# Optimization experiments

Measured on AMD Instinct MI355X. Metric: run time of the kernel, lower is better.

The kernel has to match this reference:

```python
import jax, jax.numpy as jnp
import numpy as np
from jax import lax

N, H, W = 16, 112, 112
CIN, COUT, K = 256, 256, 3
STRIDE, PAD = 1, 1


def setup_inputs() -> dict:
    key = jax.random.key(0)
    kx, kw = jax.random.split(key)
    # int8-valued activations and weights, stored as int32 for portable integer conv
    x = jax.random.randint(kx, (N, H, W, CIN), -128, 128, dtype=jnp.int32)
    # weight layout matches the torch module: (out_channels, kH, kW, in_channels) == OHWI
    weight = jax.random.randint(kw, (COUT, K, K, CIN), -128, 128, dtype=jnp.int32)
    return {"x": x, "weight": weight}


def reference(x, weight):
    y = lax.conv_general_dilated(
        x,
        weight,
        window_strides=(STRIDE, STRIDE),
        padding=[(PAD, PAD), (PAD, PAD)],
        dimension_numbers=("NHWC", "OHWI", "NHWC"),
        preferred_element_type=jnp.int32,
    )
    return y  # (N, H, W, COUT) int32
```

## Files before the change

### kernel.cpp

```cpp
#include <hip/hip_runtime.h>
#include <stdint.h>

#define NN   16
#define HH   112
#define WW   112
#define CIN  256
#define COUT 256
#define HP   114
#define WP   114
#define M_TOTAL (NN * HH * WW)
#define XP_BYTES ((size_t)NN * HP * WP * CIN)
#define WPK_BYTES ((size_t)9 * COUT * CIN)

typedef int v4i __attribute__((ext_vector_type(4)));

__device__ __forceinline__ void load_lds16(const void* g, void* l) {
  __builtin_amdgcn_global_load_lds(
      (const __attribute__((address_space(1))) void*)g,
      (__attribute__((address_space(3))) void*)l, 16, 0, 0);
}

__device__ __forceinline__ void bar() {
  asm volatile("" ::: "memory");
  __builtin_amdgcn_s_barrier();
  asm volatile("" ::: "memory");
}

__device__ __forceinline__ int pack4(int a, int b, int c, int d) {
  return (a & 255) | ((b & 255) << 8) | ((c & 255) << 16) | (d << 24);
}

__global__ void pack_x_kernel(const int* __restrict__ x, char* __restrict__ xp) {
  int t = blockIdx.x * 256 + threadIdx.x;
  int g = t & 15;
  int p = t >> 4;
  int w = p % WW;
  int t2 = p / WW;
  int h = t2 % HH;
  int n = t2 / HH;
  const int4* src = (const int4*)(x + (size_t)t * 16);
  int4 a = src[0], b = src[1], c = src[2], d = src[3];
  int4 ov;
  ov.x = pack4(a.x, a.y, a.z, a.w);
  ov.y = pack4(b.x, b.y, b.z, b.w);
  ov.z = pack4(c.x, c.y, c.z, c.w);
  ov.w = pack4(d.x, d.y, d.z, d.w);
  size_t dst = (((size_t)n * HP + (h + 1)) * WP + (w + 1)) * CIN + (size_t)g * 16;
  *(int4*)(xp + dst) = ov;
}

__global__ void pack_w_border_kernel(const int* __restrict__ wgt, char* __restrict__ xp,
                                     char* __restrict__ wp) {
  int bid = blockIdx.x;
  if (bid < 576) {
    int t = bid * 256 + threadIdx.x;
    int c4 = t & 63;
    int r = t >> 6;
    int tap = r % 9;
    int cout = r / 9;
    int4 v = *(const int4*)(wgt + (size_t)t * 4);
    int ov = pack4(v.x, v.y, v.z, v.w);
    size_t dst = ((size_t)tap * COUT + cout) * CIN + (size_t)c4 * 4;
    *(int*)(wp + dst) = ov;
  } else {
    int t = (bid - 576) * 256 + threadIdx.x;
    int g = t & 15;
    int pix = t >> 4;
    int n = pix / 452;
    int b = pix % 452;
    int h, w;
    if (b < 114) { h = 0; w = b; }
    else if (b < 228) { h = 113; w = b - 114; }
    else { int r = b - 228; h = 1 + (r >> 1); w = (r & 1) ? 113 : 0; }
    size_t dst = (((size_t)n * HP + h) * WP + w) * CIN + (size_t)g * 16;
    *(int4*)(xp + dst) = make_int4(0, 0, 0, 0);
  }
}

__global__ __launch_bounds__(256, 2) void conv_mfma_kernel(const char* __restrict__ xp,
                                                           const char* __restrict__ wp,
                                                           int* __restrict__ out) {
  __shared__ __align__(16) char Bs[3 * 256 * 64];
  const int tid = threadIdx.x;
  const int lane = tid & 63;
  const int wave = tid >> 6;
  const int mtile = blockIdx.x;
  const int wm = wave & 1;
  const int wn = wave >> 1;

  const char* gptrB[4];
  char* lptrB[4];
#pragma unroll
  for (int j = 0; j < 4; j++) {
    int c = wave * 4 + j;
    int row = c * 16 + (lane >> 2);
    int colg = (lane & 3) ^ ((row >> 1) & 3);
    gptrB[j] = wp + (size_t)row * CIN + (size_t)colg * 16;
    lptrB[j] = Bs + c * 1024;
  }

  const char* abase[4];
#pragma unroll
  for (int i = 0; i < 4; i++) {
    int ra = mtile * 128 + wm * 64 + i * 16 + (lane & 15);
    int w = ra % WW;
    int t2 = ra / WW;
    int h = t2 % HH;
    int n = t2 / HH;
    abase[i] = xp + (((size_t)n * HP + h) * WP + w) * CIN + (size_t)(lane >> 4) * 16;
  }

  int boff[8];
#pragma unroll
  for (int j = 0; j < 8; j++) {
    int rb = wn * 128 + j * 16 + (lane & 15);
    boff[j] = rb * 64 + (((lane >> 4) ^ ((rb >> 1) & 3)) * 16);
  }

  v4i acc[4][8];
#pragma unroll
  for (int i = 0; i < 4; i++)
#pragma unroll
    for (int j = 0; j < 8; j++) acc[i][j] = (v4i){0, 0, 0, 0};

  auto stageB = [&](int ks, int b) {
    int tap = ks >> 2;
    int kb = ks & 3;
    int offB = tap * (COUT * CIN) + kb * 64;
#pragma unroll
    for (int j = 0; j < 4; j++) load_lds16(gptrB[j] + offB, lptrB[j] + b * 16384);
  };
  auto gatherA = [&](int ks, v4i* dst) {
    int tap = ks >> 2;
    int kb = ks & 3;
    int ky = tap / 3;
    int kx = tap - ky * 3;
    int off = (ky * WP + kx) * CIN + kb * 64;
#pragma unroll
    for (int i = 0; i < 4; i++) dst[i] = *(const v4i*)(abase[i] + off);
  };

  v4i afr[2][4];

  stageB(0, 0);
  stageB(1, 1);
  gatherA(0, afr[0]);
  asm volatile("s_waitcnt vmcnt(8)" ::: "memory");
  bar();

#define CONV_STEP(KS, BC, CUR, NXT, DOSTAGE, DOGATHER, VMN)                         \
  {                                                                                 \
    const char* Bb = Bs + (BC) * 16384;                                             \
    v4i bf[8];                                                                      \
    _Pragma("unroll") for (int j = 0; j < 8; j++)                                   \
        bf[j] = *(const v4i*)(Bb + boff[j]);                                        \
    if (DOSTAGE) stageB((KS) + 2, ((BC) + 2) % 3);                                  \
    if (DOGATHER) gatherA((KS) + 1, afr[NXT]);                                      \
    asm volatile("s_waitcnt vmcnt(" VMN ")" ::: "memory");                          \
    __builtin_amdgcn_s_setprio(1);                                                  \
    _Pragma("unroll") for (int i = 0; i < 4; i++)                                   \
      _Pragma("unroll") for (int j = 0; j < 8; j++)                                 \
        acc[i][j] = __builtin_amdgcn_mfma_i32_16x16x64_i8(afr[CUR][i], bf[j],       \
                                                          acc[i][j], 0, 0, 0);      \
    __builtin_amdgcn_s_setprio(0);                                                  \
    bar();                                                                          \
  }

#pragma unroll 1
  for (int it = 0; it < 5; it++) {
    int base = it * 6;
#pragma unroll
    for (int u = 0; u < 6; u++) {
      CONV_STEP(base + u, u % 3, u & 1, (u + 1) & 1, true, true, "8")
    }
  }
  CONV_STEP(30, 0, 0, 1, true,  true,  "8")
  CONV_STEP(31, 1, 1, 0, true,  true,  "8")
  CONV_STEP(32, 2, 0, 1, true,  true,  "8")
  CONV_STEP(33, 0, 1, 0, true,  true,  "8")
  CONV_STEP(34, 1, 0, 1, false, true,  "4")
  CONV_STEP(35, 2, 1, 0, false, false, "0")
#undef CONV_STEP

#pragma unroll
  for (int i = 0; i < 4; i++) {
    const int mg = mtile * 128 + wm * 64 + i * 16 + ((lane >> 4) * 4);
#pragma unroll
    for (int r = 0; r < 4; r++) {
      int* orow = out + (size_t)(mg + r) * COUT + wn * 128 + (lane & 15);
#pragma unroll
      for (int j = 0; j < 8; j++) orow[j * 16] = acc[i][j][r];
    }
  }
}

__global__ void conv_naive_kernel(const int* __restrict__ x, const int* __restrict__ wgt,
                                  int* __restrict__ out, int total) {
  int idx = blockIdx.x * 256 + threadIdx.x;
  if (idx >= total) return;
  int co = idx & 255;
  int p = idx >> 8;
  int w = p % WW;
  int t2 = p / WW;
  int h = t2 % HH;
  int n = t2 / HH;
  int acc = 0;
  for (int ky = 0; ky < 3; ky++) {
    int ih = h + ky - 1;
    if (ih < 0 || ih >= HH) continue;
    for (int kx = 0; kx < 3; kx++) {
      int iw = w + kx - 1;
      if (iw < 0 || iw >= WW) continue;
      const int* xs = x + (((size_t)n * HH + ih) * WW + iw) * CIN;
      const int* ws = wgt + ((size_t)co * 9 + ky * 3 + kx) * CIN;
      for (int ci = 0; ci < CIN; ci++) acc += xs[ci] * ws[ci];
    }
  }
  out[idx] = acc;
}

extern "C" void kernel_launch(void* const* d_in, const int* in_sizes, int n_in,
                              void* d_out, int out_size, void* d_ws, size_t ws_size,
                              hipStream_t stream) {
  const int* x = (const int*)d_in[0];
  const int* wgt = (const int*)d_in[1];
  int* out = (int*)d_out;
  const size_t need = XP_BYTES + WPK_BYTES;
  if (ws_size >= need) {
    char* xp = (char*)d_ws;
    char* wp = xp + XP_BYTES;
    pack_x_kernel<<<(M_TOTAL * 16) / 256, 256, 0, stream>>>(x, xp);
    pack_w_border_kernel<<<576 + 452, 256, 0, stream>>>(wgt, xp, wp);
    conv_mfma_kernel<<<M_TOTAL / 128, 256, 0, stream>>>(xp, wp, out);
  } else {
    conv_naive_kernel<<<(out_size + 255) / 256, 256, 0, stream>>>(x, wgt, out, out_size);
  }
}
```

Baseline: 571.3 us.

## Enlarge conv tile to 256x256 with LDS-staged A and 4-deep pipeline

The conv kernel moves from 128-row tiles with 4 waves to 256-row by 256-column tiles with 8 waves. Both the im2col A tile and the B weights are now staged into LDS with direct global-to-LDS loads through a 4-buffer ring, replacing per-lane global gathers of A. Each wave computes 128x64 in two halves with extra barriers between them. The two pack kernels are merged into one launch. The aim is more data reuse per block and less global A traffic, at the cost of more LDS use (128KB), more barriers and possibly lower occupancy.

Result: faster. 473.1 us (-17.2%).

```diff
diff --git a/kernel.cpp b/kernel.cpp
--- a/kernel.cpp
+++ b/kernel.cpp
@@ -20,40 +20,34 @@
       (__attribute__((address_space(3))) void*)l, 16, 0, 0);
 }
 
-__device__ __forceinline__ void bar() {
-  asm volatile("" ::: "memory");
-  __builtin_amdgcn_s_barrier();
-  asm volatile("" ::: "memory");
-}
-
 __device__ __forceinline__ int pack4(int a, int b, int c, int d) {
   return (a & 255) | ((b & 255) << 8) | ((c & 255) << 16) | (d << 24);
 }
 
-__global__ void pack_x_kernel(const int* __restrict__ x, char* __restrict__ xp) {
-  int t = blockIdx.x * 256 + threadIdx.x;
-  int g = t & 15;
-  int p = t >> 4;
-  int w = p % WW;
-  int t2 = p / WW;
-  int h = t2 % HH;
-  int n = t2 / HH;
-  const int4* src = (const int4*)(x + (size_t)t * 16);
-  int4 a = src[0], b = src[1], c = src[2], d = src[3];
-  int4 ov;
-  ov.x = pack4(a.x, a.y, a.z, a.w);
-  ov.y = pack4(b.x, b.y, b.z, b.w);
-  ov.z = pack4(c.x, c.y, c.z, c.w);
-  ov.w = pack4(d.x, d.y, d.z, d.w);
-  size_t dst = (((size_t)n * HP + (h + 1)) * WP + (w + 1)) * CIN + (size_t)g * 16;
-  *(int4*)(xp + dst) = ov;
-}
-
-__global__ void pack_w_border_kernel(const int* __restrict__ wgt, char* __restrict__ xp,
-                                     char* __restrict__ wp) {
+__global__ __launch_bounds__(256) void pack_all_kernel(const int* __restrict__ x,
+                                                       const int* __restrict__ wgt,
+                                                       char* __restrict__ xp,
+                                                       char* __restrict__ wp) {
   int bid = blockIdx.x;
-  if (bid < 576) {
+  if (bid < 12544) {
     int t = bid * 256 + threadIdx.x;
+    int g = t & 15;
+    int p = t >> 4;
+    int w = p % WW;
+    int t2 = p / WW;
+    int h = t2 % HH;
+    int n = t2 / HH;
+    const int4* src = (const int4*)(x + (size_t)t * 16);
+    int4 a = src[0], b = src[1], c = src[2], d = src[3];
+    int4 ov;
+    ov.x = pack4(a.x, a.y, a.z, a.w);
+    ov.y = pack4(b.x, b.y, b.z, b.w);
+    ov.z = pack4(c.x, c.y, c.z, c.w);
+    ov.w = pack4(d.x, d.y, d.z, d.w);
+    size_t dst = (((size_t)n * HP + (h + 1)) * WP + (w + 1)) * CIN + (size_t)g * 16;
+    *(int4*)(xp + dst) = ov;
+  } else if (bid < 12544 + 576) {
+    int t = (bid - 12544) * 256 + threadIdx.x;
     int c4 = t & 63;
     int r = t >> 6;
     int tap = r % 9;
@@ -63,7 +57,7 @@
     size_t dst = ((size_t)tap * COUT + cout) * CIN + (size_t)c4 * 4;
     *(int*)(wp + dst) = ov;
   } else {
-    int t = (bid - 576) * 256 + threadIdx.x;
+    int t = (bid - 13120) * 256 + threadIdx.x;
     int g = t & 15;
     int pix = t >> 4;
     int n = pix / 452;
@@ -77,10 +71,11 @@
   }
 }
 
-__global__ __launch_bounds__(256, 2) void conv_mfma_kernel(const char* __restrict__ xp,
+__global__ __launch_bounds__(512, 2) void conv_mfma_kernel(const char* __restrict__ xp,
                                                            const char* __restrict__ wp,
                                                            int* __restrict__ out) {
-  __shared__ __align__(16) char Bs[3 * 256 * 64];
+  __shared__ __align__(16) char As[4 * 16384];
+  __shared__ __align__(16) char Bs[4 * 16384];
   const int tid = threadIdx.x;
   const int lane = tid & 63;
   const int wave = tid >> 6;
@@ -88,108 +83,121 @@
   const int wm = wave & 1;
   const int wn = wave >> 1;
 
-  const char* gptrB[4];
-  char* lptrB[4];
+  const int rA0 = (tid >> 2);
+  const int rA1 = 128 + (tid >> 2);
+  const int gcA0 = (tid & 3) ^ ((rA0 >> 1) & 3);
+  const int gcA1 = (tid & 3) ^ ((rA1 >> 1) & 3);
+  const char *gsrcA0, *gsrcA1;
+  {
+    int m0 = mtile * 256 + rA0;
+    int w0 = m0 % WW; int q0 = m0 / WW; int h0 = q0 % HH; int n0 = q0 / HH;
+    gsrcA0 = xp + (((size_t)n0 * HP + h0) * WP + w0) * CIN + (size_t)gcA0 * 16;
+    int m1 = mtile * 256 + rA1;
+    int w1 = m1 % WW; int q1 = m1 / WW; int h1 = q1 % HH; int n1 = q1 / HH;
+    gsrcA1 = xp + (((size_t)n1 * HP + h1) * WP + w1) * CIN + (size_t)gcA1 * 16;
+  }
+  const char* gsrcB0 = wp + (size_t)rA0 * CIN + (size_t)gcA0 * 16;
+  const char* gsrcB1 = wp + (size_t)rA1 * CIN + (size_t)gcA1 * 16;
+
+  int aoff[8], boff[4];
+#pragma unroll
+  for (int i = 0; i < 8; i++) {
+    int r = wm * 128 + i * 16 + (lane & 15);
+    aoff[i] = r * 64 + (((lane >> 4) ^ ((r >> 1) & 3)) * 16);
+  }
 #pragma unroll
   for (int j = 0; j < 4; j++) {
-    int c = wave * 4 + j;
-    int row = c * 16 + (lane >> 2);
-    int colg = (lane & 3) ^ ((row >> 1) & 3);
-    gptrB[j] = wp + (size_t)row * CIN + (size_t)colg * 16;
-    lptrB[j] = Bs + c * 1024;
-  }
-
-  const char* abase[4];
-#pragma unroll
-  for (int i = 0; i < 4; i++) {
-    int ra = mtile * 128 + wm * 64 + i * 16 + (lane & 15);
-    int w = ra % WW;
-    int t2 = ra / WW;
-    int h = t2 % HH;
-    int n = t2 / HH;
-    abase[i] = xp + (((size_t)n * HP + h) * WP + w) * CIN + (size_t)(lane >> 4) * 16;
-  }
-
-  int boff[8];
-#pragma unroll
-  for (int j = 0; j < 8; j++) {
-    int rb = wn * 128 + j * 16 + (lane & 15);
+    int rb = wn * 64 + j * 16 + (lane & 15);
     boff[j] = rb * 64 + (((lane >> 4) ^ ((rb >> 1) & 3)) * 16);
   }
 
-  v4i acc[4][8];
-#pragma unroll
-  for (int i = 0; i < 4; i++)
-#pragma unroll
-    for (int j = 0; j < 8; j++) acc[i][j] = (v4i){0, 0, 0, 0};
-
-  auto stageB = [&](int ks, int b) {
-    int tap = ks >> 2;
-    int kb = ks & 3;
-    int offB = tap * (COUT * CIN) + kb * 64;
-#pragma unroll
-    for (int j = 0; j < 4; j++) load_lds16(gptrB[j] + offB, lptrB[j] + b * 16384);
+  v4i acc[8][4];
+#pragma unroll
+  for (int i = 0; i < 8; i++)
+#pragma unroll
+    for (int j = 0; j < 4; j++) acc[i][j] = (v4i){0, 0, 0, 0};
+
+  auto stage = [&](int oA, int oB, int buf) {
+    char* Adst = As + buf * 16384 + wave * 1024;
+    char* Bdst = Bs + buf * 16384 + wave * 1024;
+    load_lds16(gsrcA0 + oA, Adst);
+    load_lds16(gsrcA1 + oA, Adst + 8192);
+    load_lds16(gsrcB0 + oB, Bdst);
+    load_lds16(gsrcB1 + oB, Bdst + 8192);
   };
-  auto gatherA = [&](int ks, v4i* dst) {
-    int tap = ks >> 2;
-    int kb = ks & 3;
-    int ky = tap / 3;
-    int kx = tap - ky * 3;
-    int off = (ky * WP + kx) * CIN + kb * 64;
-#pragma unroll
-    for (int i = 0; i < 4; i++) dst[i] = *(const v4i*)(abase[i] + off);
-  };
-
-  v4i afr[2][4];
-
-  stageB(0, 0);
-  stageB(1, 1);
-  gatherA(0, afr[0]);
+
+  stage(0, 0, 0);
+  stage(64, 64, 1);
+  stage(128, 128, 2);
   asm volatile("s_waitcnt vmcnt(8)" ::: "memory");
-  bar();
-
-#define CONV_STEP(KS, BC, CUR, NXT, DOSTAGE, DOGATHER, VMN)                         \
+  __builtin_amdgcn_s_barrier();
+
+#define CONV_STEP(U, SOA, SOB, DOSTAGE, VMN)                                        \
   {                                                                                 \
-    const char* Bb = Bs + (BC) * 16384;                                             \
-    v4i bf[8];                                                                      \
-    _Pragma("unroll") for (int j = 0; j < 8; j++)                                   \
+    const char* Ab = As + (U) * 16384;                                              \
+    const char* Bb = Bs + (U) * 16384;                                              \
+    v4i af[4], bf[4], af2[4];                                                       \
+                                  \
+    _Pragma("unroll") for (int i = 0; i < 4; i++)                                   \
+        af[i] = *(const v4i*)(Ab + aoff[i]);                                        \
+    _Pragma("unroll") for (int j = 0; j < 4; j++)                                   \
         bf[j] = *(const v4i*)(Bb + boff[j]);                                        \
-    if (DOSTAGE) stageB((KS) + 2, ((BC) + 2) % 3);                                  \
-    if (DOGATHER) gatherA((KS) + 1, afr[NXT]);                                      \
-    asm volatile("s_waitcnt vmcnt(" VMN ")" ::: "memory");                          \
+    if (DOSTAGE) stage((SOA), (SOB), ((U) + 3) & 3);                                \
+    __builtin_amdgcn_s_barrier();                                                   \
+    asm volatile("s_waitcnt lgkmcnt(0)" ::: "memory");                              \
     __builtin_amdgcn_s_setprio(1);                                                  \
     _Pragma("unroll") for (int i = 0; i < 4; i++)                                   \
-      _Pragma("unroll") for (int j = 0; j < 8; j++)                                 \
-        acc[i][j] = __builtin_amdgcn_mfma_i32_16x16x64_i8(afr[CUR][i], bf[j],       \
+      _Pragma("unroll") for (int j = 0; j < 4; j++)                                 \
+        acc[i][j] = __builtin_amdgcn_mfma_i32_16x16x64_i8(af[i], bf[j],             \
                                                           acc[i][j], 0, 0, 0);      \
     __builtin_amdgcn_s_setprio(0);                                                  \
-    bar();                                                                          \
+    __builtin_amdgcn_s_barrier();                                                   \
+               \
+    _Pragma("unroll") for (int i = 0; i < 4; i++)                                   \
+        af2[i] = *(const v4i*)(Ab + aoff[4 + i]);                                   \
+    __builtin_amdgcn_s_barrier();                                                   \
+    asm volatile("s_waitcnt lgkmcnt(0)" ::: "memory");                              \
+    __builtin_amdgcn_s_setprio(1);                                                  \
+    _Pragma("unroll") for (int i = 0; i < 4; i++)                                   \
+      _Pragma("unroll") for (int j = 0; j < 4; j++)                                 \
+        acc[4 + i][j] = __builtin_amdgcn_mfma_i32_16x16x64_i8(af2[i], bf[j],        \
+                                                              acc[4 + i][j], 0, 0, 0); \
+    __builtin_amdgcn_s_setprio(0);                                                  \
+    asm volatile("s_waitcnt vmcnt(" VMN ")" ::: "memory");                          \
+    __builtin_amdgcn_s_barrier();                                                   \
   }
 
 #pragma unroll 1
-  for (int it = 0; it < 5; it++) {
-    int base = it * 6;
-#pragma unroll
-    for (int u = 0; u < 6; u++) {
-      CONV_STEP(base + u, u % 3, u & 1, (u + 1) & 1, true, true, "8")
-    }
-  }
-  CONV_STEP(30, 0, 0, 1, true,  true,  "8")
-  CONV_STEP(31, 1, 1, 0, true,  true,  "8")
-  CONV_STEP(32, 2, 0, 1, true,  true,  "8")
-  CONV_STEP(33, 0, 1, 0, true,  true,  "8")
-  CONV_STEP(34, 1, 0, 1, false, true,  "4")
-  CONV_STEP(35, 2, 1, 0, false, false, "0")
+  for (int g = 0; g < 8; g++) {
+    int ky0 = g / 3, kx0 = g - ky0 * 3;
+    int oA0 = (ky0 * WP + kx0) * CIN;
+    int oB0 = g * (COUT * CIN);
+    int ky1 = (g + 1) / 3, kx1 = (g + 1) - ky1 * 3;
+    int oA1 = (ky1 * WP + kx1) * CIN;
+    int oB1 = (g + 1) * (COUT * CIN);
+    CONV_STEP(0, oA0 + 192, oB0 + 192, true, "8")
+    CONV_STEP(1, oA1,       oB1,       true, "8")
+    CONV_STEP(2, oA1 + 64,  oB1 + 64,  true, "8")
+    CONV_STEP(3, oA1 + 128, oB1 + 128, true, "8")
+  }
+  {
+    int oA8 = (2 * WP + 2) * CIN;
+    int oB8 = 8 * (COUT * CIN);
+    CONV_STEP(0, oA8 + 192, oB8 + 192, true,  "8")
+    CONV_STEP(1, 0, 0, false, "4")
+    CONV_STEP(2, 0, 0, false, "0")
+    CONV_STEP(3, 0, 0, false, "0")
+  }
 #undef CONV_STEP
 
 #pragma unroll
-  for (int i = 0; i < 4; i++) {
-    const int mg = mtile * 128 + wm * 64 + i * 16 + ((lane >> 4) * 4);
+  for (int i = 0; i < 8; i++) {
+    const int mg = mtile * 256 + wm * 128 + i * 16 + ((lane >> 4) * 4);
 #pragma unroll
     for (int r = 0; r < 4; r++) {
-      int* orow = out + (size_t)(mg + r) * COUT + wn * 128 + (lane & 15);
-#pragma unroll
-      for (int j = 0; j < 8; j++) orow[j * 16] = acc[i][j][r];
+      int* orow = out + (size_t)(mg + r) * COUT + wn * 64 + (lane & 15);
+#pragma unroll
+      for (int j = 0; j < 4; j++) orow[j * 16] = acc[i][j][r];
     }
   }
 }
@@ -229,9 +237,8 @@
   if (ws_size >= need) {
     char* xp = (char*)d_ws;
     char* wp = xp + XP_BYTES;
-    pack_x_kernel<<<(M_TOTAL * 16) / 256, 256, 0, stream>>>(x, xp);
-    pack_w_border_kernel<<<576 + 452, 256, 0, stream>>>(wgt, xp, wp);
-    conv_mfma_kernel<<<M_TOTAL / 128, 256, 0, stream>>>(xp, wp, out);
+    pack_all_kernel<<<13572, 256, 0, stream>>>(x, wgt, xp, wp);
+    conv_mfma_kernel<<<M_TOTAL / 256, 512, 0, stream>>>(xp, wp, out);
   } else {
     conv_naive_kernel<<<(out_size + 255) / 256, 256, 0, stream>>>(x, wgt, out, out_size);
   }
```

## Stage activations in LDS and read pre-swizzled weights directly from global

Applied to the files above, without the earlier changes.

Swaps the roles of the operands. The im2col activation tile is now staged into a 4-deep LDS ring with async global-to-LDS loads, and the weights are repacked into an MFMA-fragment-ready layout that each wave reads straight from global memory (cached in L2). The two pack kernels are merged into one launch, which removes a launch boundary. This cuts LDS footprint and per-wave gather addressing, but the B fragment loads now go to global or L2 on the critical path before each MFMA group, and the vmcnt wait placement changes.

Result: faster. 474.1 us (-17.0%).

```diff
diff --git a/kernel.cpp b/kernel.cpp
--- a/kernel.cpp
+++ b/kernel.cpp
@@ -20,50 +20,48 @@
       (__attribute__((address_space(3))) void*)l, 16, 0, 0);
 }
 
-__device__ __forceinline__ void bar() {
-  asm volatile("" ::: "memory");
-  __builtin_amdgcn_s_barrier();
-  asm volatile("" ::: "memory");
-}
-
 __device__ __forceinline__ int pack4(int a, int b, int c, int d) {
   return (a & 255) | ((b & 255) << 8) | ((c & 255) << 16) | (d << 24);
 }
 
-__global__ void pack_x_kernel(const int* __restrict__ x, char* __restrict__ xp) {
-  int t = blockIdx.x * 256 + threadIdx.x;
-  int g = t & 15;
-  int p = t >> 4;
-  int w = p % WW;
-  int t2 = p / WW;
-  int h = t2 % HH;
-  int n = t2 / HH;
-  const int4* src = (const int4*)(x + (size_t)t * 16);
-  int4 a = src[0], b = src[1], c = src[2], d = src[3];
-  int4 ov;
-  ov.x = pack4(a.x, a.y, a.z, a.w);
-  ov.y = pack4(b.x, b.y, b.z, b.w);
-  ov.z = pack4(c.x, c.y, c.z, c.w);
-  ov.w = pack4(d.x, d.y, d.z, d.w);
-  size_t dst = (((size_t)n * HP + (h + 1)) * WP + (w + 1)) * CIN + (size_t)g * 16;
-  *(int4*)(xp + dst) = ov;
-}
-
-__global__ void pack_w_border_kernel(const int* __restrict__ wgt, char* __restrict__ xp,
-                                     char* __restrict__ wp) {
+__global__ __launch_bounds__(256) void pack_all_kernel(const int* __restrict__ x,
+                                                       const int* __restrict__ wgt,
+                                                       char* __restrict__ xp,
+                                                       char* __restrict__ wp) {
   int bid = blockIdx.x;
-  if (bid < 576) {
+  if (bid < 12544) {
     int t = bid * 256 + threadIdx.x;
-    int c4 = t & 63;
-    int r = t >> 6;
-    int tap = r % 9;
-    int cout = r / 9;
-    int4 v = *(const int4*)(wgt + (size_t)t * 4);
+    int g = t & 15;
+    int p = t >> 4;
+    int w = p % WW;
+    int t2 = p / WW;
+    int h = t2 % HH;
+    int n = t2 / HH;
+    const int4* src = (const int4*)(x + (size_t)t * 16);
+    int4 a = src[0], b = src[1], c = src[2], d = src[3];
+    int4 ov;
+    ov.x = pack4(a.x, a.y, a.z, a.w);
+    ov.y = pack4(b.x, b.y, b.z, b.w);
+    ov.z = pack4(c.x, c.y, c.z, c.w);
+    ov.w = pack4(d.x, d.y, d.z, d.w);
+    size_t dst = (((size_t)n * HP + (h + 1)) * WP + (w + 1)) * CIN + (size_t)g * 16;
+    *(int4*)(xp + dst) = ov;
+  } else if (bid < 12544 + 576) {
+    int t = (bid - 12544) * 256 + threadIdx.x;
+    int i = t * 4;
+    int cout = i / 2304;
+    int rem = i - cout * 2304;
+    int tap = rem >> 8;
+    int ci = rem & 255;
+    int4 v = *(const int4*)(wgt + (size_t)i);
     int ov = pack4(v.x, v.y, v.z, v.w);
-    size_t dst = ((size_t)tap * COUT + cout) * CIN + (size_t)c4 * 4;
+    int kb = ci >> 6;
+    int jg = cout >> 4;
+    int l = ((ci >> 4) & 3) * 16 + (cout & 15);
+    size_t dst = (((size_t)(tap * 4 + kb) * 16 + jg) * 1024) + (size_t)l * 16 + (ci & 15);
     *(int*)(wp + dst) = ov;
   } else {
-    int t = (bid - 576) * 256 + threadIdx.x;
+    int t = (bid - 13120) * 256 + threadIdx.x;
     int g = t & 15;
     int pix = t >> 4;
     int n = pix / 452;
@@ -78,9 +76,9 @@
 }
 
 __global__ __launch_bounds__(256, 2) void conv_mfma_kernel(const char* __restrict__ xp,
-                                                           const char* __restrict__ wp,
+                                                           const char* __restrict__ wp2,
                                                            int* __restrict__ out) {
-  __shared__ __align__(16) char Bs[3 * 256 * 64];
+  __shared__ __align__(16) char As[4 * 8192];
   const int tid = threadIdx.x;
   const int lane = tid & 63;
   const int wave = tid >> 6;
@@ -88,33 +86,27 @@
   const int wm = wave & 1;
   const int wn = wave >> 1;
 
-  const char* gptrB[4];
-  char* lptrB[4];
-#pragma unroll
-  for (int j = 0; j < 4; j++) {
-    int c = wave * 4 + j;
-    int row = c * 16 + (lane >> 2);
-    int colg = (lane & 3) ^ ((row >> 1) & 3);
-    gptrB[j] = wp + (size_t)row * CIN + (size_t)colg * 16;
-    lptrB[j] = Bs + c * 1024;
-  }
-
-  const char* abase[4];
-#pragma unroll
-  for (int i = 0; i < 4; i++) {
-    int ra = mtile * 128 + wm * 64 + i * 16 + (lane & 15);
-    int w = ra % WW;
-    int t2 = ra / WW;
+  const char* gsrcA[2];
+#pragma unroll
+  for (int q = 0; q < 2; q++) {
+    int p = wave * 2048 + q * 1024 + lane * 16;
+    int row = p >> 6;
+    int colg = ((p >> 4) & 3) ^ ((row >> 1) & 3);
+    int m = mtile * 128 + row;
+    int w = m % WW;
+    int t2 = m / WW;
     int h = t2 % HH;
     int n = t2 / HH;
-    abase[i] = xp + (((size_t)n * HP + h) * WP + w) * CIN + (size_t)(lane >> 4) * 16;
-  }
-
-  int boff[8];
-#pragma unroll
-  for (int j = 0; j < 8; j++) {
-    int rb = wn * 128 + j * 16 + (lane & 15);
-    boff[j] = rb * 64 + (((lane >> 4) ^ ((rb >> 1) & 3)) * 16);
+    gsrcA[q] = xp + (((size_t)n * HP + h) * WP + w) * CIN + (size_t)colg * 16;
+  }
+
+  const char* bptr = wp2 + (size_t)(wn * 8) * 1024 + (size_t)lane * 16;
+
+  int aoff[4];
+#pragma unroll
+  for (int i = 0; i < 4; i++) {
+    int r = wm * 64 + i * 16 + (lane & 15);
+    aoff[i] = r * 64 + (((lane >> 4) ^ ((r >> 1) & 3)) * 16);
   }
 
   v4i acc[4][8];
@@ -123,63 +115,64 @@
 #pragma unroll
     for (int j = 0; j < 8; j++) acc[i][j] = (v4i){0, 0, 0, 0};
 
-  auto stageB = [&](int ks, int b) {
-    int tap = ks >> 2;
-    int kb = ks & 3;
-    int offB = tap * (COUT * CIN) + kb * 64;
-#pragma unroll
-    for (int j = 0; j < 4; j++) load_lds16(gptrB[j] + offB, lptrB[j] + b * 16384);
-  };
-  auto gatherA = [&](int ks, v4i* dst) {
-    int tap = ks >> 2;
-    int kb = ks & 3;
+  auto stageA = [&](int s, int buf) {
+    int tap = s >> 2;
+    int kb = s & 3;
     int ky = tap / 3;
     int kx = tap - ky * 3;
     int off = (ky * WP + kx) * CIN + kb * 64;
-#pragma unroll
-    for (int i = 0; i < 4; i++) dst[i] = *(const v4i*)(abase[i] + off);
+    load_lds16(gsrcA[0] + off, As + buf * 8192 + wave * 2048);
+    load_lds16(gsrcA[1] + off, As + buf * 8192 + wave * 2048 + 1024);
   };
 
-  v4i afr[2][4];
-
-  stageB(0, 0);
-  stageB(1, 1);
-  gatherA(0, afr[0]);
-  asm volatile("s_waitcnt vmcnt(8)" ::: "memory");
-  bar();
-
-#define CONV_STEP(KS, BC, CUR, NXT, DOSTAGE, DOGATHER, VMN)                         \
+  stageA(0, 0);
+  stageA(1, 1);
+  asm volatile("s_waitcnt vmcnt(2)" ::: "memory");
+  __builtin_amdgcn_s_barrier();
+
+#define CONV_STEP(BUF, SB, DOSTAGE, SOA, SBUF, VMN)                                 \
   {                                                                                 \
-    const char* Bb = Bs + (BC) * 16384;                                             \
+    const char* Ab = As + (BUF) * 8192;                                             \
     v4i bf[8];                                                                      \
     _Pragma("unroll") for (int j = 0; j < 8; j++)                                   \
-        bf[j] = *(const v4i*)(Bb + boff[j]);                                        \
-    if (DOSTAGE) stageB((KS) + 2, ((BC) + 2) % 3);                                  \
-    if (DOGATHER) gatherA((KS) + 1, afr[NXT]);                                      \
-    asm volatile("s_waitcnt vmcnt(" VMN ")" ::: "memory");                          \
+        bf[j] = *(const v4i*)(bptr + (size_t)(SB) * 16384 + j * 1024);              \
+    v4i af[4];                                                                      \
+    _Pragma("unroll") for (int i = 0; i < 4; i++)                                   \
+        af[i] = *(const v4i*)(Ab + aoff[i]);                                        \
+    __builtin_amdgcn_sched_barrier(0);                                              \
+    if (DOSTAGE) {                                                                  \
+      load_lds16(gsrcA[0] + (SOA), As + (SBUF) * 8192 + wave * 2048);               \
+      load_lds16(gsrcA[1] + (SOA), As + (SBUF) * 8192 + wave * 2048 + 1024);        \
+    }                                                                               \
     __builtin_amdgcn_s_setprio(1);                                                  \
     _Pragma("unroll") for (int i = 0; i < 4; i++)                                   \
       _Pragma("unroll") for (int j = 0; j < 8; j++)                                 \
-        acc[i][j] = __builtin_amdgcn_mfma_i32_16x16x64_i8(afr[CUR][i], bf[j],       \
+        acc[i][j] = __builtin_amdgcn_mfma_i32_16x16x64_i8(af[i], bf[j],             \
                                                           acc[i][j], 0, 0, 0);      \
     __builtin_amdgcn_s_setprio(0);                                                  \
-    bar();                                                                          \
+    asm volatile("s_waitcnt vmcnt(" VMN ")" ::: "memory");                          \
+    __builtin_amdgcn_s_barrier();                                                   \
   }
 
 #pragma unroll 1
-  for (int it = 0; it < 5; it++) {
-    int base = it * 6;
-#pragma unroll
-    for (int u = 0; u < 6; u++) {
-      CONV_STEP(base + u, u % 3, u & 1, (u + 1) & 1, true, true, "8")
-    }
-  }
-  CONV_STEP(30, 0, 0, 1, true,  true,  "8")
-  CONV_STEP(31, 1, 1, 0, true,  true,  "8")
-  CONV_STEP(32, 2, 0, 1, true,  true,  "8")
-  CONV_STEP(33, 0, 1, 0, true,  true,  "8")
-  CONV_STEP(34, 1, 0, 1, false, true,  "4")
-  CONV_STEP(35, 2, 1, 0, false, false, "0")
+  for (int g = 0; g < 8; g++) {
+    int ky0 = g / 3, kx0 = g - ky0 * 3;
+    int oA0 = (ky0 * WP + kx0) * CIN;
+    int ky1 = (g + 1) / 3, kx1 = (g + 1) - ky1 * 3;
+    int oA1 = (ky1 * WP + kx1) * CIN;
+    int sb = 4 * g;
+    CONV_STEP(0, sb + 0, true, oA0 + 128, 2, "2")
+    CONV_STEP(1, sb + 1, true, oA0 + 192, 3, "2")
+    CONV_STEP(2, sb + 2, true, oA1 + 0,   0, "2")
+    CONV_STEP(3, sb + 3, true, oA1 + 64,  1, "2")
+  }
+  {
+    int oA8 = (2 * WP + 2) * CIN;
+    CONV_STEP(0, 32, true,  oA8 + 128, 2, "2")
+    CONV_STEP(1, 33, true,  oA8 + 192, 3, "2")
+    CONV_STEP(2, 34, false, 0, 0, "0")
+    CONV_STEP(3, 35, false, 0, 0, "0")
+  }
 #undef CONV_STEP
 
 #pragma unroll
@@ -229,8 +222,7 @@
   if (ws_size >= need) {
     char* xp = (char*)d_ws;
     char* wp = xp + XP_BYTES;
-    pack_x_kernel<<<(M_TOTAL * 16) / 256, 256, 0, stream>>>(x, xp);
-    pack_w_border_kernel<<<576 + 452, 256, 0, stream>>>(wgt, xp, wp);
+    pack_all_kernel<<<13572, 256, 0, stream>>>(x, wgt, xp, wp);
     conv_mfma_kernel<<<M_TOTAL / 128, 256, 0, stream>>>(xp, wp, out);
   } else {
     conv_naive_kernel<<<(out_size + 255) / 256, 256, 0, stream>>>(x, wgt, out, out_size);
```
